# Performance work log

Measured on AMD Instinct MI355X. Metric: run time of the kernel, lower is better.

The kernel has to match this reference:

```python
import jax, jax.numpy as jnp
import numpy as np

N_NODES = 50000
N_EDGES = 800000
ND = 64   # node_dim
HD = 128  # hidden_dim
ED = 32   # edge_dim


def setup_inputs() -> dict:
    key = jax.random.key(0)
    ks = jax.random.split(key, 16)
    init = lambda k, shape: (jax.random.normal(k, shape, jnp.float32)
                             / np.float32(np.sqrt(shape[0])))
    h = jax.random.normal(ks[0], (N_NODES, ND), jnp.float32)
    x = jax.random.normal(ks[1], (N_NODES, 3), jnp.float32) * 10.0
    edge_index = jax.random.randint(ks[2], (2, N_EDGES), 0, N_NODES, dtype=jnp.int64)
    # realistic edge distances = actual pairwise distances of sampled edges
    edge_dist = jnp.linalg.norm(x[edge_index[0]] - x[edge_index[1]], axis=-1)
    in_dim = 2 * ND + ED
    return {
        "h": h, "x": x, "edge_index": edge_index, "edge_dist": edge_dist,
        # edge_mlp: Linear(1, ED) -> SiLU -> Linear(ED, ED)
        "We1": init(ks[3], (1, ED)), "be1": jnp.zeros((ED,), jnp.float32),
        "We2": init(ks[4], (ED, ED)), "be2": jnp.zeros((ED,), jnp.float32),
        # node_mlp: Linear(in_dim, HD) -> SiLU -> Linear(HD, ND)
        "Wn1": init(ks[5], (in_dim, HD)), "bn1": jnp.zeros((HD,), jnp.float32),
        "Wn2": init(ks[6], (HD, ND)), "bn2": jnp.zeros((ND,), jnp.float32),
        # coord_mlp: Linear(in_dim, HD) -> SiLU -> Linear(HD, 1, bias=False)
        "Wc1": init(ks[7], (in_dim, HD)), "bc1": jnp.zeros((HD,), jnp.float32),
        "Wc2": init(ks[8], (HD, 1)),
    }


def reference(h, x, edge_index, edge_dist,
              We1, be1, We2, be2,
              Wn1, bn1, Wn2, bn2,
              Wc1, bc1, Wc2):
    n = h.shape[0]
    src, dst = edge_index[0], edge_index[1]
    # edge_mlp on scalar distance -> [E, ED]
    e = jax.nn.silu(edge_dist[:, None] @ We1 + be1) @ We2 + be2
    # gather + concat -> [E, 2*ND + ED]
    m_input = jnp.concatenate([h[src], h[dst], e], axis=-1)
    # node messages [E, ND]
    m = jax.nn.silu(m_input @ Wn1 + bn1) @ Wn2 + bn2
    h_agg = jax.ops.segment_sum(m, dst, num_segments=n)
    # coord update weight [E, 1]
    coord_weight = jax.nn.silu(m_input @ Wc1 + bc1) @ Wc2
    dir_vec = x[src] - x[dst]
    dir_len = jnp.clip(jnp.linalg.norm(dir_vec, axis=-1, keepdims=True), 1e-8)
    coord_update = coord_weight * (dir_vec / dir_len)
    x_agg = jax.ops.segment_sum(coord_update, dst, num_segments=n)
    return h + h_agg, x + x_agg
```

## Files before the change

### kernel.cpp

```cpp
#include <hip/hip_runtime.h>


#define NN 50000
#define NE 800000
#define NDIM 64
#define HDIM 128
#define EDIM 32
#define NTILES (NE / 64)
#define MSTRIDE 168
#define HSTRIDE 136
#define MLSTRIDE 65
#define NH (NN * NDIM)
#define NX (NN * 3)

#define WS_WN1P 0
#define WS_WC1P 20480
#define WS_BN1P 40960
#define WS_BC1P 41088
#define WS_WEIGHTS_FLOATS 65536
#define NCNT 50176
#define IOFF_CNT    WS_WEIGHTS_FLOATS
#define IOFF_BLK    (IOFF_CNT + NCNT)
#define IOFF_CUR    (IOFF_BLK + 256)
#define IOFF_SRCS   (IOFF_CUR + NCNT)
#define IOFF_DSTS   (IOFF_SRCS + NE)
#define IOFF_DISTS  (IOFF_DSTS + NE)
#define WS_TOTAL_BYTES ((size_t)(IOFF_DISTS + NE) * 4)

typedef __bf16 bf16x8 __attribute__((ext_vector_type(8)));
typedef float f32x4 __attribute__((ext_vector_type(4)));
typedef unsigned short ushort8 __attribute__((ext_vector_type(8)));
typedef unsigned short ushort4v __attribute__((ext_vector_type(4)));

__device__ __forceinline__ unsigned short f2bf(float f) {
    union { __bf16 b; unsigned short u; } c;
    c.b = (__bf16)f;
    return c.u;
}
__device__ __forceinline__ float silu(float v) {
    return __fdividef(v, 1.0f + __expf(-v));
}

__device__ __forceinline__ void bar_lds() {
    asm volatile("s_waitcnt lgkmcnt(0)" ::: "memory");
    __builtin_amdgcn_s_barrier();
}

__device__ __forceinline__ bf16x8 ld_frag(const unsigned short* p) {
    union { ushort8 u; bf16x8 v; } c;
    c.u = *(const ushort8*)p;
    return c.v;
}
__device__ __forceinline__ bf16x8 mk_frag(const unsigned short* u) {
    union { ushort8 uu; bf16x8 v; } c;
#pragma unroll
    for (int j = 0; j < 8; ++j) c.uu[j] = u[j];
    return c.v;
}

__global__ void init_out(const float* __restrict__ h, const float* __restrict__ x,
                         float* __restrict__ out) {
    int i = blockIdx.x * 256 + threadIdx.x;
    if (i < NH) out[i] = h[i];
    else if (i < NH + NX) out[i] = x[i - NH];
}


__global__ __launch_bounds__(256) void zero_cnt(int* __restrict__ cnt, int* __restrict__ cur) {
    const int i = blockIdx.x * 256 + threadIdx.x;
    if (i < NCNT) { cnt[i] = 0; cur[i] = 0; }
}

__global__ __launch_bounds__(256) void hist_dst(const int* __restrict__ dst, int* __restrict__ cnt) {
    const int e = blockIdx.x * 256 + threadIdx.x;
    if (e < NE) atomicAdd(&cnt[dst[e]], 1);
}

__global__ __launch_bounds__(256) void scan1(int* __restrict__ cnt, int* __restrict__ blk) {
    __shared__ int sh[256];
    const int t = threadIdx.x, i = blockIdx.x * 256 + t;
    const int v = cnt[i];
    sh[t] = v;
    __syncthreads();
#pragma unroll
    for (int d = 1; d < 256; d <<= 1) {
        const int o = (t >= d) ? sh[t - d] : 0;
        __syncthreads();
        sh[t] += o;
        __syncthreads();
    }
    cnt[i] = sh[t] - v;
    if (t == 255) blk[blockIdx.x] = sh[t];
}

__global__ __launch_bounds__(256) void scan2(int* __restrict__ blk) {
    __shared__ int sh[256];
    const int t = threadIdx.x;
    const int v = (t < 196) ? blk[t] : 0;
    sh[t] = v;
    __syncthreads();
#pragma unroll
    for (int d = 1; d < 256; d <<= 1) {
        const int o = (t >= d) ? sh[t - d] : 0;
        __syncthreads();
        sh[t] += o;
        __syncthreads();
    }
    if (t < 196) blk[t] = sh[t] - v;
}

__global__ __launch_bounds__(256) void scan3(int* __restrict__ cnt, const int* __restrict__ blk) {
    const int i = blockIdx.x * 256 + threadIdx.x;
    if (i < NCNT) cnt[i] += blk[blockIdx.x];
}

__global__ __launch_bounds__(256) void scatter_edges(
    const int* __restrict__ src, const int* __restrict__ dst,
    const float* __restrict__ dist,
    const int* __restrict__ base, int* __restrict__ cur,
    int* __restrict__ srcs, int* __restrict__ dsts, float* __restrict__ dists) {
    const int e = blockIdx.x * 256 + threadIdx.x;
    if (e < NE) {
        const int d = dst[e];
        const int pos = base[d] + atomicAdd(&cur[d], 1);
        srcs[pos] = src[e];
        dsts[pos] = d;
        dists[pos] = dist[e];
    }
}


__global__ __launch_bounds__(128) void fold_weights(
    const float* __restrict__ We2, const float* __restrict__ be2,
    const float* __restrict__ Wn1, const float* __restrict__ bn1,
    const float* __restrict__ Wc1, const float* __restrict__ bc1,
    float* __restrict__ ws) {
    const int b = blockIdx.x;
    const int col = threadIdx.x;
    if (b < 320) {
        const int path = (b >= 160);
        const float* W = path ? Wc1 : Wn1;
        float* Wp = ws + (path ? WS_WC1P : WS_WN1P);
        const int r = path ? (b - 160) : b;
        if (r < 128) {
            Wp[r * 128 + col] = W[r * 128 + col];
        } else {
            const int j = r - 128;
            float s = 0.0f;
#pragma unroll
            for (int n = 0; n < 32; ++n)
                s += We2[j * 32 + n] * W[(128 + n) * 128 + col];
            Wp[r * 128 + col] = s;
        }
    } else {
        const int path = b - 320;
        const float* W = path ? Wc1 : Wn1;
        const float* bb = path ? bc1 : bn1;
        float* bp = ws + (path ? WS_BC1P : WS_BN1P);
        float s = bb[col];
#pragma unroll
        for (int n = 0; n < 32; ++n)
            s += be2[n] * W[(128 + n) * 128 + col];
        bp[col] = s;
    }
}


__global__ __launch_bounds__(256, 2) void egnn_edges(
    const float* __restrict__ h, const float* __restrict__ x,
    const int* __restrict__ srcg, const int* __restrict__ dstg,
    const float* __restrict__ dist,
    const float* __restrict__ We1, const float* __restrict__ be1,
    const float* __restrict__ Wn2, const float* __restrict__ bn2,
    const float* __restrict__ Wc2,
    const float* __restrict__ wsW,
    float* __restrict__ outh, float* __restrict__ outx) {

    __shared__ __align__(16) unsigned short mlds[64 * MSTRIDE];
    __shared__ __align__(16) unsigned short hl[64 * HSTRIDE];
    __shared__ int src_l[64];
    __shared__ int dst_l[64];
    __shared__ float we1_l[32], be1_l[32];
    __shared__ float part_l[256];
    __shared__ float cx_l[64], cy_l[64], cz_l[64];

    const int tid  = threadIdx.x;
    const int w    = tid >> 6;
    const int lane = tid & 63;
    const int l15  = lane & 15;
    const int quad = lane >> 4;

    const float* Wn1p = wsW + WS_WN1P;
    const float* Wc1p = wsW + WS_WC1P;
    const float* bn1p = wsW + WS_BN1P;
    const float* bc1p = wsW + WS_BC1P;

    if (tid < 32) { we1_l[tid] = We1[tid]; be1_l[tid] = be1[tid]; }

    bf16x8 wn1f[5][2], wc1f[5][2];
#pragma unroll
    for (int kc = 0; kc < 5; ++kc) {
#pragma unroll
        for (int nt = 0; nt < 2; ++nt) {
            unsigned short un[8], uc[8];
            const int n = w * 32 + nt * 16 + l15;
#pragma unroll
            for (int j = 0; j < 8; ++j) {
                const int k = kc * 32 + quad * 8 + j;
                un[j] = f2bf(Wn1p[k * HDIM + n]);
                uc[j] = f2bf(Wc1p[k * HDIM + n]);
            }
            wn1f[kc][nt] = mk_frag(un);
            wc1f[kc][nt] = mk_frag(uc);
        }
    }
    bf16x8 wn2f[4];
#pragma unroll
    for (int kc = 0; kc < 4; ++kc) {
        unsigned short u[8];
        const int n = w * 16 + l15;
#pragma unroll
        for (int j = 0; j < 8; ++j) {
            const int k = kc * 32 + quad * 8 + j;
            u[j] = f2bf(Wn2[k * NDIM + n]);
        }
        wn2f[kc] = mk_frag(u);
    }
    const float biasN0 = bn1p[w * 32 + l15];
    const float biasN1 = bn1p[w * 32 + 16 + l15];
    const float biasC0 = bc1p[w * 32 + l15];
    const float biasC1 = bc1p[w * 32 + 16 + l15];
    const float bias2v = bn2[w * 16 + l15];
    const float wcA = Wc2[w * 32 + l15];
    const float wcB = Wc2[w * 32 + 16 + l15];

    for (int tile = blockIdx.x; tile < NTILES; tile += gridDim.x) {
        int pf_s = 0, pf_d = 0;
        if (tid < 64) {
            const int e = tile * 64 + tid;
            pf_s = srcg[e];
            pf_d = dstg[e];
        }
        bar_lds();

        if (tid < 64) { src_l[tid] = pf_s; dst_l[tid] = pf_d; }
        bar_lds();

        {
            const int c4 = tid & 15, sub = tid >> 4;
#pragma unroll
            for (int it = 0; it < 4; ++it) {
                const int el = sub + it * 16;
                const float4 hs = *(const float4*)(h + (size_t)src_l[el] * NDIM + c4 * 4);
                const float4 hd = *(const float4*)(h + (size_t)dst_l[el] * NDIM + c4 * 4);
                ushort4v us = { f2bf(hs.x), f2bf(hs.y), f2bf(hs.z), f2bf(hs.w) };
                ushort4v ud = { f2bf(hd.x), f2bf(hd.y), f2bf(hd.z), f2bf(hd.w) };
                *(ushort4v*)&mlds[el * MSTRIDE + c4 * 4] = us;
                *(ushort4v*)&mlds[el * MSTRIDE + 64 + c4 * 4] = ud;
            }
        }
        {
            const int el = tid >> 2, j0 = (tid & 3) * 8;
            const float dv = dist[tile * 64 + el];
            ushort8 u;
#pragma unroll
            for (int j = 0; j < 8; ++j)
                u[j] = f2bf(silu(dv * we1_l[j0 + j] + be1_l[j0 + j]));
            *(ushort8*)&mlds[el * MSTRIDE + 128 + j0] = u;
        }
        bar_lds();

        f32x4 accN[4][2], accC[4][2];
#pragma unroll
        for (int mt = 0; mt < 4; ++mt) {
            accN[mt][0] = (f32x4){biasN0, biasN0, biasN0, biasN0};
            accN[mt][1] = (f32x4){biasN1, biasN1, biasN1, biasN1};
            accC[mt][0] = (f32x4){biasC0, biasC0, biasC0, biasC0};
            accC[mt][1] = (f32x4){biasC1, biasC1, biasC1, biasC1};
        }
#pragma unroll
        for (int kc = 0; kc < 5; ++kc) {
            bf16x8 af[4];
#pragma unroll
            for (int mt = 0; mt < 4; ++mt)
                af[mt] = ld_frag(&mlds[(mt * 16 + l15) * MSTRIDE + kc * 32 + quad * 8]);
#pragma unroll
            for (int mt = 0; mt < 4; ++mt) {
#pragma unroll
                for (int nt = 0; nt < 2; ++nt) {
                    accN[mt][nt] = __builtin_amdgcn_mfma_f32_16x16x32_bf16(
                        af[mt], wn1f[kc][nt], accN[mt][nt], 0, 0, 0);
                    accC[mt][nt] = __builtin_amdgcn_mfma_f32_16x16x32_bf16(
                        af[mt], wc1f[kc][nt], accC[mt][nt], 0, 0, 0);
                }
            }
        }

#pragma unroll
        for (int mt = 0; mt < 4; ++mt)
#pragma unroll
            for (int nt = 0; nt < 2; ++nt)
#pragma unroll
                for (int r = 0; r < 4; ++r)
                    hl[(mt * 16 + quad * 4 + r) * HSTRIDE + w * 32 + nt * 16 + l15] =
                        f2bf(silu(accN[mt][nt][r]));

        {
            float p[16];
#pragma unroll
            for (int mt = 0; mt < 4; ++mt)
#pragma unroll
                for (int r = 0; r < 4; ++r)
                    p[mt * 4 + r] = silu(accC[mt][0][r]) * wcA + silu(accC[mt][1][r]) * wcB;

            float q8[8];
#pragma unroll
            for (int i = 0; i < 8; ++i) {
                const float send = (l15 & 8) ? p[i] : p[i + 8];
                const float recv = __shfl_xor(send, 8, 64);
                q8[i] = ((l15 & 8) ? p[i + 8] : p[i]) + recv;
            }
            float q4[4];
#pragma unroll
            for (int i = 0; i < 4; ++i) {
                const float send = (l15 & 4) ? q8[i] : q8[i + 4];
                const float recv = __shfl_xor(send, 4, 64);
                q4[i] = ((l15 & 4) ? q8[i + 4] : q8[i]) + recv;
            }
            float q2[2];
#pragma unroll
            for (int i = 0; i < 2; ++i) {
                const float send = (l15 & 2) ? q4[i] : q4[i + 2];
                const float recv = __shfl_xor(send, 2, 64);
                q2[i] = ((l15 & 2) ? q4[i + 2] : q4[i]) + recv;
            }
            {
                const float send = (l15 & 1) ? q2[0] : q2[1];
                const float recv = __shfl_xor(send, 1, 64);
                const float tot = ((l15 & 1) ? q2[1] : q2[0]) + recv;
                const int edge = (l15 >> 2) * 16 + quad * 4 + (l15 & 3);
                part_l[w * 64 + edge] = tot;
            }
        }
        bar_lds();

        f32x4 acc2[4];
#pragma unroll
        for (int mt = 0; mt < 4; ++mt) acc2[mt] = (f32x4){bias2v, bias2v, bias2v, bias2v};
#pragma unroll
        for (int kc = 0; kc < 4; ++kc) {
#pragma unroll
            for (int mt = 0; mt < 4; ++mt) {
                bf16x8 a2 = ld_frag(&hl[(mt * 16 + l15) * HSTRIDE + kc * 32 + quad * 8]);
                acc2[mt] = __builtin_amdgcn_mfma_f32_16x16x32_bf16(a2, wn2f[kc], acc2[mt], 0, 0, 0);
            }
        }

        {
            float* ml = (float*)mlds;
#pragma unroll
            for (int mt = 0; mt < 4; ++mt)
#pragma unroll
                for (int r = 0; r < 4; ++r)
                    ml[(mt * 16 + quad * 4 + r) * MLSTRIDE + w * 16 + l15] = acc2[mt][r];
        }

        if (tid < 64) {
            const float cw = part_l[tid] + part_l[64 + tid] + part_l[128 + tid] + part_l[192 + tid];
            const int sn = src_l[tid], dn = dst_l[tid];
            const float dx = x[sn * 3 + 0] - x[dn * 3 + 0];
            const float dy = x[sn * 3 + 1] - x[dn * 3 + 1];
            const float dz = x[sn * 3 + 2] - x[dn * 3 + 2];
            float len = sqrtf(dx * dx + dy * dy + dz * dz);
            len = fmaxf(len, 1e-8f);
            const float f = cw / len;
            cx_l[tid] = f * dx; cy_l[tid] = f * dy; cz_l[tid] = f * dz;
        }
        bar_lds();

        {
            const int c = lane, g = w;
            const int r0 = g * 16;
            float acc = ((const float*)mlds)[r0 * MLSTRIDE + c];
            int d = dst_l[r0];
#pragma unroll
            for (int r = r0 + 1; r < r0 + 16; ++r) {
                const int dn = dst_l[r];
                if (dn != d) {
                    atomicAdd(outh + (size_t)d * NDIM + c, acc);
                    acc = 0.0f;
                    d = dn;
                }
                acc += ((const float*)mlds)[r * MLSTRIDE + c];
            }
            atomicAdd(outh + (size_t)d * NDIM + c, acc);
        }

        if (tid < 64) {
            const int d = dst_l[tid];
            if (tid == 0 || dst_l[tid - 1] != d) {
                float sx = 0.0f, sy = 0.0f, sz = 0.0f;
                int r = tid;
                do {
                    sx += cx_l[r]; sy += cy_l[r]; sz += cz_l[r];
                    ++r;
                } while (r < 64 && dst_l[r] == d);
                atomicAdd(outx + (size_t)d * 3 + 0, sx);
                atomicAdd(outx + (size_t)d * 3 + 1, sy);
                atomicAdd(outx + (size_t)d * 3 + 2, sz);
            }
        }
    }
}

extern "C" void kernel_launch(void* const* d_in, const int* in_sizes, int n_in,
                              void* d_out, int out_size, void* d_ws, size_t ws_size,
                              hipStream_t stream) {
    const float* h    = (const float*)d_in[0];
    const float* x    = (const float*)d_in[1];
    const int*   ei   = (const int*)d_in[2];
    const float* dist = (const float*)d_in[3];
    const float* We1  = (const float*)d_in[4];
    const float* be1  = (const float*)d_in[5];
    const float* We2  = (const float*)d_in[6];
    const float* be2  = (const float*)d_in[7];
    const float* Wn1  = (const float*)d_in[8];
    const float* bn1  = (const float*)d_in[9];
    const float* Wn2  = (const float*)d_in[10];
    const float* bn2  = (const float*)d_in[11];
    const float* Wc1  = (const float*)d_in[12];
    const float* bc1  = (const float*)d_in[13];
    const float* Wc2  = (const float*)d_in[14];

    float* outh = (float*)d_out;
    float* outx = outh + (size_t)NH;
    float* ws   = (float*)d_ws;

    fold_weights<<<322, 128, 0, stream>>>(We2, be2, Wn1, bn1, Wc1, bc1, ws);
    init_out<<<(NH + NX + 255) / 256, 256, 0, stream>>>(h, x, (float*)d_out);

    const int* es = ei;
    const int* ed = ei + NE;
    const float* edist = dist;

    if (ws_size >= WS_TOTAL_BYTES) {
        int*   cnt   = (int*)d_ws + IOFF_CNT;
        int*   blk   = (int*)d_ws + IOFF_BLK;
        int*   cur   = (int*)d_ws + IOFF_CUR;
        int*   srcs  = (int*)d_ws + IOFF_SRCS;
        int*   dsts  = (int*)d_ws + IOFF_DSTS;
        float* dists = (float*)((int*)d_ws + IOFF_DISTS);

        zero_cnt<<<NCNT / 256, 256, 0, stream>>>(cnt, cur);
        hist_dst<<<NE / 256, 256, 0, stream>>>(ed, cnt);
        scan1<<<NCNT / 256, 256, 0, stream>>>(cnt, blk);
        scan2<<<1, 256, 0, stream>>>(blk);
        scan3<<<NCNT / 256, 256, 0, stream>>>(cnt, blk);
        scatter_edges<<<NE / 256, 256, 0, stream>>>(es, ed, dist, cnt, cur,
                                                    srcs, dsts, dists);
        es = srcs; ed = dsts; edist = dists;
    }

    egnn_edges<<<1024, 256, 0, stream>>>(h, x, es, ed, edist,
                                         We1, be1, Wn2, bn2, Wc2, ws,
                                         outh, outx);
}
```

Measured before the change: 458.0 us.

## Fuse preprocessing kernels into one persistent prep kernel with grid sync

Replaces the weight-fold, output init, zeroing, histogram, three-stage scan and scatter kernels with a single 512-block kernel that separates its phases with atomic-counter grid barriers, plus one memset. The main edge kernel splits the node and coord first-layer MFMA loops so fewer accumulators are live, raises the occupancy hint to 3 blocks per SM, and uses a grid of 768. It also drops the separate index staging barrier by reading edge indices straight from global memory. The software grid barrier assumes all 512 blocks are resident at once and can deadlock if they are not. The extra occupancy may force register spills.

```diff
diff --git a/kernel.cpp b/kernel.cpp
--- a/kernel.cpp
+++ b/kernel.cpp
@@ -5,7 +5,6 @@
 #define NE 800000
 #define NDIM 64
 #define HDIM 128
-#define EDIM 32
 #define NTILES (NE / 64)
 #define MSTRIDE 168
 #define HSTRIDE 136
@@ -20,12 +19,17 @@
 #define WS_WEIGHTS_FLOATS 65536
 #define NCNT 50176
 #define IOFF_CNT    WS_WEIGHTS_FLOATS
-#define IOFF_BLK    (IOFF_CNT + NCNT)
-#define IOFF_CUR    (IOFF_BLK + 256)
-#define IOFF_SRCS   (IOFF_CUR + NCNT)
+#define IOFF_CUR    (IOFF_CNT + NCNT)
+#define IOFF_SYNC   (IOFF_CUR + NCNT)
+#define IOFF_BLK    (IOFF_SYNC + 64)
+#define IOFF_SRCS   (IOFF_BLK + 256)
 #define IOFF_DSTS   (IOFF_SRCS + NE)
 #define IOFF_DISTS  (IOFF_DSTS + NE)
 #define WS_TOTAL_BYTES ((size_t)(IOFF_DISTS + NE) * 4)
+#define MEMSET_OFF_BYTES ((size_t)IOFF_CNT * 4)
+#define MEMSET_BYTES ((size_t)(2 * NCNT + 64 + 256) * 4)
+
+#define PREP_NB 512
 
 typedef __bf16 bf16x8 __attribute__((ext_vector_type(8)));
 typedef float f32x4 __attribute__((ext_vector_type(4)));
@@ -40,12 +44,10 @@
 __device__ __forceinline__ float silu(float v) {
     return __fdividef(v, 1.0f + __expf(-v));
 }
-
 __device__ __forceinline__ void bar_lds() {
     asm volatile("s_waitcnt lgkmcnt(0)" ::: "memory");
     __builtin_amdgcn_s_barrier();
 }
-
 __device__ __forceinline__ bf16x8 ld_frag(const unsigned short* p) {
     union { ushort8 u; bf16x8 v; } c;
     c.u = *(const ushort8*)p;
@@ -58,115 +60,129 @@
     return c.v;
 }
 
-__global__ void init_out(const float* __restrict__ h, const float* __restrict__ x,
-                         float* __restrict__ out) {
-    int i = blockIdx.x * 256 + threadIdx.x;
-    if (i < NH) out[i] = h[i];
-    else if (i < NH + NX) out[i] = x[i - NH];
-}
-
-
-__global__ __launch_bounds__(256) void zero_cnt(int* __restrict__ cnt, int* __restrict__ cur) {
-    const int i = blockIdx.x * 256 + threadIdx.x;
-    if (i < NCNT) { cnt[i] = 0; cur[i] = 0; }
-}
-
-__global__ __launch_bounds__(256) void hist_dst(const int* __restrict__ dst, int* __restrict__ cnt) {
-    const int e = blockIdx.x * 256 + threadIdx.x;
-    if (e < NE) atomicAdd(&cnt[dst[e]], 1);
-}
-
-__global__ __launch_bounds__(256) void scan1(int* __restrict__ cnt, int* __restrict__ blk) {
-    __shared__ int sh[256];
-    const int t = threadIdx.x, i = blockIdx.x * 256 + t;
-    const int v = cnt[i];
-    sh[t] = v;
+
+__device__ __forceinline__ void gsync(int* sc) {
     __syncthreads();
-#pragma unroll
-    for (int d = 1; d < 256; d <<= 1) {
-        const int o = (t >= d) ? sh[t - d] : 0;
-        __syncthreads();
-        sh[t] += o;
-        __syncthreads();
-    }
-    cnt[i] = sh[t] - v;
-    if (t == 255) blk[blockIdx.x] = sh[t];
-}
-
-__global__ __launch_bounds__(256) void scan2(int* __restrict__ blk) {
-    __shared__ int sh[256];
-    const int t = threadIdx.x;
-    const int v = (t < 196) ? blk[t] : 0;
-    sh[t] = v;
+    if (threadIdx.x == 0) {
+        __threadfence();
+        atomicAdd(sc, 1);
+        while (__hip_atomic_load(sc, __ATOMIC_RELAXED, __HIP_MEMORY_SCOPE_AGENT) < PREP_NB)
+            __builtin_amdgcn_s_sleep(2);
+        __threadfence();
+    }
     __syncthreads();
-#pragma unroll
-    for (int d = 1; d < 256; d <<= 1) {
-        const int o = (t >= d) ? sh[t - d] : 0;
-        __syncthreads();
-        sh[t] += o;
-        __syncthreads();
-    }
-    if (t < 196) blk[t] = sh[t] - v;
-}
-
-__global__ __launch_bounds__(256) void scan3(int* __restrict__ cnt, const int* __restrict__ blk) {
-    const int i = blockIdx.x * 256 + threadIdx.x;
-    if (i < NCNT) cnt[i] += blk[blockIdx.x];
-}
-
-__global__ __launch_bounds__(256) void scatter_edges(
-    const int* __restrict__ src, const int* __restrict__ dst,
-    const float* __restrict__ dist,
-    const int* __restrict__ base, int* __restrict__ cur,
-    int* __restrict__ srcs, int* __restrict__ dsts, float* __restrict__ dists) {
-    const int e = blockIdx.x * 256 + threadIdx.x;
-    if (e < NE) {
-        const int d = dst[e];
-        const int pos = base[d] + atomicAdd(&cur[d], 1);
-        srcs[pos] = src[e];
-        dsts[pos] = d;
-        dists[pos] = dist[e];
-    }
-}
-
-
-__global__ __launch_bounds__(128) void fold_weights(
+}
+
+__global__ __launch_bounds__(256) void prep(
+    const float* __restrict__ h, const float* __restrict__ x,
+    const int* __restrict__ src0, const int* __restrict__ dst0,
+    const float* __restrict__ dist0,
     const float* __restrict__ We2, const float* __restrict__ be2,
     const float* __restrict__ Wn1, const float* __restrict__ bn1,
     const float* __restrict__ Wc1, const float* __restrict__ bc1,
-    float* __restrict__ ws) {
-    const int b = blockIdx.x;
-    const int col = threadIdx.x;
-    if (b < 320) {
-        const int path = (b >= 160);
-        const float* W = path ? Wc1 : Wn1;
-        float* Wp = ws + (path ? WS_WC1P : WS_WN1P);
-        const int r = path ? (b - 160) : b;
-        if (r < 128) {
-            Wp[r * 128 + col] = W[r * 128 + col];
+    float* __restrict__ out, int* __restrict__ wsi, int do_sort) {
+
+    __shared__ int sh[256];
+    const int gtid = blockIdx.x * 256 + threadIdx.x;
+    const int G = PREP_NB * 256;
+
+    float* wsf = (float*)wsi;
+    int* cnt  = wsi + IOFF_CNT;
+    int* cur  = wsi + IOFF_CUR;
+    int* sync = wsi + IOFF_SYNC;
+    int* blk  = wsi + IOFF_BLK;
+
+    for (int i = gtid; i < 41216; i += G) {
+        if (i < 40960) {
+            const int path = i / 20480;
+            const int rem = i - path * 20480;
+            const int r = rem >> 7, col = rem & 127;
+            const float* W = path ? Wc1 : Wn1;
+            float* Wp = wsf + (path ? WS_WC1P : WS_WN1P);
+            if (r < 128) {
+                Wp[r * 128 + col] = W[r * 128 + col];
+            } else {
+                const int j = r - 128;
+                float s = 0.0f;
+#pragma unroll
+                for (int n = 0; n < 32; ++n)
+                    s += We2[j * 32 + n] * W[(128 + n) * 128 + col];
+                Wp[r * 128 + col] = s;
+            }
         } else {
-            const int j = r - 128;
-            float s = 0.0f;
+            const int j = i - 40960;
+            const int path = j >> 7, col = j & 127;
+            const float* W = path ? Wc1 : Wn1;
+            const float* bb = path ? bc1 : bn1;
+            float s = bb[col];
 #pragma unroll
             for (int n = 0; n < 32; ++n)
-                s += We2[j * 32 + n] * W[(128 + n) * 128 + col];
-            Wp[r * 128 + col] = s;
-        }
-    } else {
-        const int path = b - 320;
-        const float* W = path ? Wc1 : Wn1;
-        const float* bb = path ? bc1 : bn1;
-        float* bp = ws + (path ? WS_BC1P : WS_BN1P);
-        float s = bb[col];
-#pragma unroll
-        for (int n = 0; n < 32; ++n)
-            s += be2[n] * W[(128 + n) * 128 + col];
-        bp[col] = s;
-    }
-}
-
-
-__global__ __launch_bounds__(256, 2) void egnn_edges(
+                s += be2[n] * W[(128 + n) * 128 + col];
+            wsf[(path ? WS_BC1P : WS_BN1P) + col] = s;
+        }
+    }
+    for (int i = gtid; i < NH + NX; i += G)
+        out[i] = (i < NH) ? h[i] : x[i - NH];
+
+    if (!do_sort) return;
+
+    gsync(&sync[0]);
+
+    for (int e = gtid; e < NE; e += G)
+        atomicAdd(&cnt[dst0[e]], 1);
+
+    gsync(&sync[16]);
+
+    if (blockIdx.x < 196) {
+        const int t = threadIdx.x;
+        const int i = blockIdx.x * 256 + t;
+        const int v = cnt[i];
+        sh[t] = v;
+        __syncthreads();
+#pragma unroll
+        for (int d = 1; d < 256; d <<= 1) {
+            const int o = (t >= d) ? sh[t - d] : 0;
+            __syncthreads();
+            sh[t] += o;
+            __syncthreads();
+        }
+        cnt[i] = sh[t] - v;
+        if (t == 255) blk[blockIdx.x] = sh[t];
+    }
+
+    gsync(&sync[32]);
+
+    if (blockIdx.x == 0) {
+        const int t = threadIdx.x;
+        const int v = (t < 196) ? blk[t] : 0;
+        sh[t] = v;
+        __syncthreads();
+#pragma unroll
+        for (int d = 1; d < 256; d <<= 1) {
+            const int o = (t >= d) ? sh[t - d] : 0;
+            __syncthreads();
+            sh[t] += o;
+            __syncthreads();
+        }
+        if (t < 196) blk[t] = sh[t] - v;
+    }
+
+    gsync(&sync[48]);
+
+    int* srcs = wsi + IOFF_SRCS;
+    int* dsts = wsi + IOFF_DSTS;
+    float* dists = (float*)(wsi + IOFF_DISTS);
+    for (int e = gtid; e < NE; e += G) {
+        const int d = dst0[e];
+        const int pos = cnt[d] + blk[d >> 8] + atomicAdd(&cur[d], 1);
+        srcs[pos] = src0[e];
+        dsts[pos] = d;
+        dists[pos] = dist0[e];
+    }
+}
+
+
+__global__ __launch_bounds__(256, 3) void egnn_edges(
     const float* __restrict__ h, const float* __restrict__ x,
     const int* __restrict__ srcg, const int* __restrict__ dstg,
     const float* __restrict__ dist,
@@ -235,24 +251,19 @@
     const float wcB = Wc2[w * 32 + 16 + l15];
 
     for (int tile = blockIdx.x; tile < NTILES; tile += gridDim.x) {
-        int pf_s = 0, pf_d = 0;
-        if (tid < 64) {
-            const int e = tile * 64 + tid;
-            pf_s = srcg[e];
-            pf_d = dstg[e];
-        }
+        const int e0 = tile * 64;
         bar_lds();
 
-        if (tid < 64) { src_l[tid] = pf_s; dst_l[tid] = pf_d; }
-        bar_lds();
-
+        if (tid < 64) { src_l[tid] = srcg[e0 + tid]; dst_l[tid] = dstg[e0 + tid]; }
         {
             const int c4 = tid & 15, sub = tid >> 4;
 #pragma unroll
             for (int it = 0; it < 4; ++it) {
                 const int el = sub + it * 16;
-                const float4 hs = *(const float4*)(h + (size_t)src_l[el] * NDIM + c4 * 4);
-                const float4 hd = *(const float4*)(h + (size_t)dst_l[el] * NDIM + c4 * 4);
+                const int sn = srcg[e0 + el];
+                const int dn = dstg[e0 + el];
+                const float4 hs = *(const float4*)(h + (size_t)sn * NDIM + c4 * 4);
+                const float4 hd = *(const float4*)(h + (size_t)dn * NDIM + c4 * 4);
                 ushort4v us = { f2bf(hs.x), f2bf(hs.y), f2bf(hs.z), f2bf(hs.w) };
                 ushort4v ud = { f2bf(hd.x), f2bf(hd.y), f2bf(hd.z), f2bf(hd.w) };
                 *(ushort4v*)&mlds[el * MSTRIDE + c4 * 4] = us;
@@ -261,7 +272,7 @@
         }
         {
             const int el = tid >> 2, j0 = (tid & 3) * 8;
-            const float dv = dist[tile * 64 + el];
+            const float dv = dist[e0 + el];
             ushort8 u;
 #pragma unroll
             for (int j = 0; j < 8; ++j)
@@ -270,42 +281,48 @@
         }
         bar_lds();
 
-        f32x4 accN[4][2], accC[4][2];
-#pragma unroll
-        for (int mt = 0; mt < 4; ++mt) {
-            accN[mt][0] = (f32x4){biasN0, biasN0, biasN0, biasN0};
-            accN[mt][1] = (f32x4){biasN1, biasN1, biasN1, biasN1};
-            accC[mt][0] = (f32x4){biasC0, biasC0, biasC0, biasC0};
-            accC[mt][1] = (f32x4){biasC1, biasC1, biasC1, biasC1};
-        }
-#pragma unroll
-        for (int kc = 0; kc < 5; ++kc) {
-            bf16x8 af[4];
+        {
+            f32x4 accN[4][2];
+#pragma unroll
+            for (int mt = 0; mt < 4; ++mt) {
+                accN[mt][0] = (f32x4){biasN0, biasN0, biasN0, biasN0};
+                accN[mt][1] = (f32x4){biasN1, biasN1, biasN1, biasN1};
+            }
+#pragma unroll
+            for (int kc = 0; kc < 5; ++kc) {
+#pragma unroll
+                for (int mt = 0; mt < 4; ++mt) {
+                    bf16x8 af = ld_frag(&mlds[(mt * 16 + l15) * MSTRIDE + kc * 32 + quad * 8]);
+                    accN[mt][0] = __builtin_amdgcn_mfma_f32_16x16x32_bf16(af, wn1f[kc][0], accN[mt][0], 0, 0, 0);
+                    accN[mt][1] = __builtin_amdgcn_mfma_f32_16x16x32_bf16(af, wn1f[kc][1], accN[mt][1], 0, 0, 0);
+                }
+            }
 #pragma unroll
             for (int mt = 0; mt < 4; ++mt)
-                af[mt] = ld_frag(&mlds[(mt * 16 + l15) * MSTRIDE + kc * 32 + quad * 8]);
+#pragma unroll
+                for (int nt = 0; nt < 2; ++nt)
+#pragma unroll
+                    for (int r = 0; r < 4; ++r)
+                        hl[(mt * 16 + quad * 4 + r) * HSTRIDE + w * 32 + nt * 16 + l15] =
+                            f2bf(silu(accN[mt][nt][r]));
+        }
+
+        {
+            f32x4 accC[4][2];
 #pragma unroll
             for (int mt = 0; mt < 4; ++mt) {
-#pragma unroll
-                for (int nt = 0; nt < 2; ++nt) {
-                    accN[mt][nt] = __builtin_amdgcn_mfma_f32_16x16x32_bf16(
-                        af[mt], wn1f[kc][nt], accN[mt][nt], 0, 0, 0);
-                    accC[mt][nt] = __builtin_amdgcn_mfma_f32_16x16x32_bf16(
-                        af[mt], wc1f[kc][nt], accC[mt][nt], 0, 0, 0);
+                accC[mt][0] = (f32x4){biasC0, biasC0, biasC0, biasC0};
+                accC[mt][1] = (f32x4){biasC1, biasC1, biasC1, biasC1};
+            }
+#pragma unroll
+            for (int kc = 0; kc < 5; ++kc) {
+#pragma unroll
+                for (int mt = 0; mt < 4; ++mt) {
+                    bf16x8 af = ld_frag(&mlds[(mt * 16 + l15) * MSTRIDE + kc * 32 + quad * 8]);
+                    accC[mt][0] = __builtin_amdgcn_mfma_f32_16x16x32_bf16(af, wc1f[kc][0], accC[mt][0], 0, 0, 0);
+                    accC[mt][1] = __builtin_amdgcn_mfma_f32_16x16x32_bf16(af, wc1f[kc][1], accC[mt][1], 0, 0, 0);
                 }
             }
-        }
-
-#pragma unroll
-        for (int mt = 0; mt < 4; ++mt)
-#pragma unroll
-            for (int nt = 0; nt < 2; ++nt)
-#pragma unroll
-                for (int r = 0; r < 4; ++r)
-                    hl[(mt * 16 + quad * 4 + r) * HSTRIDE + w * 32 + nt * 16 + l15] =
-                        f2bf(silu(accN[mt][nt][r]));
-
-        {
             float p[16];
 #pragma unroll
             for (int mt = 0; mt < 4; ++mt)
@@ -344,19 +361,18 @@
         }
         bar_lds();
 
-        f32x4 acc2[4];
-#pragma unroll
-        for (int mt = 0; mt < 4; ++mt) acc2[mt] = (f32x4){bias2v, bias2v, bias2v, bias2v};
-#pragma unroll
-        for (int kc = 0; kc < 4; ++kc) {
-#pragma unroll
-            for (int mt = 0; mt < 4; ++mt) {
-                bf16x8 a2 = ld_frag(&hl[(mt * 16 + l15) * HSTRIDE + kc * 32 + quad * 8]);
-                acc2[mt] = __builtin_amdgcn_mfma_f32_16x16x32_bf16(a2, wn2f[kc], acc2[mt], 0, 0, 0);
-            }
-        }
-
-        {
+        {
+            f32x4 acc2[4];
+#pragma unroll
+            for (int mt = 0; mt < 4; ++mt) acc2[mt] = (f32x4){bias2v, bias2v, bias2v, bias2v};
+#pragma unroll
+            for (int kc = 0; kc < 4; ++kc) {
+#pragma unroll
+                for (int mt = 0; mt < 4; ++mt) {
+                    bf16x8 a2 = ld_frag(&hl[(mt * 16 + l15) * HSTRIDE + kc * 32 + quad * 8]);
+                    acc2[mt] = __builtin_amdgcn_mfma_f32_16x16x32_bf16(a2, wn2f[kc], acc2[mt], 0, 0, 0);
+                }
+            }
             float* ml = (float*)mlds;
 #pragma unroll
             for (int mt = 0; mt < 4; ++mt)
@@ -379,8 +395,8 @@
         bar_lds();
 
         {
-            const int c = lane, g = w;
-            const int r0 = g * 16;
+            const int c = lane;
+            const int r0 = w * 16;
             float acc = ((const float*)mlds)[r0 * MLSTRIDE + c];
             int d = dst_l[r0];
 #pragma unroll
@@ -434,34 +450,27 @@
 
     float* outh = (float*)d_out;
     float* outx = outh + (size_t)NH;
-    float* ws   = (float*)d_ws;
-
-    fold_weights<<<322, 128, 0, stream>>>(We2, be2, Wn1, bn1, Wc1, bc1, ws);
-    init_out<<<(NH + NX + 255) / 256, 256, 0, stream>>>(h, x, (float*)d_out);
+    int*   wsi  = (int*)d_ws;
+
+    const int do_sort = (ws_size >= WS_TOTAL_BYTES) ? 1 : 0;
+    if (do_sort)
+        hipMemsetAsync((char*)d_ws + MEMSET_OFF_BYTES, 0, MEMSET_BYTES, stream);
+
+    prep<<<PREP_NB, 256, 0, stream>>>(h, x, ei, ei + NE, dist,
+                                      We2, be2, Wn1, bn1, Wc1, bc1,
+                                      (float*)d_out, wsi, do_sort);
 
     const int* es = ei;
     const int* ed = ei + NE;
     const float* edist = dist;
-
-    if (ws_size >= WS_TOTAL_BYTES) {
-        int*   cnt   = (int*)d_ws + IOFF_CNT;
-        int*   blk   = (int*)d_ws + IOFF_BLK;
-        int*   cur   = (int*)d_ws + IOFF_CUR;
-        int*   srcs  = (int*)d_ws + IOFF_SRCS;
-        int*   dsts  = (int*)d_ws + IOFF_DSTS;
-        float* dists = (float*)((int*)d_ws + IOFF_DISTS);
-
-        zero_cnt<<<NCNT / 256, 256, 0, stream>>>(cnt, cur);
-        hist_dst<<<NE / 256, 256, 0, stream>>>(ed, cnt);
-        scan1<<<NCNT / 256, 256, 0, stream>>>(cnt, blk);
-        scan2<<<1, 256, 0, stream>>>(blk);
-        scan3<<<NCNT / 256, 256, 0, stream>>>(cnt, blk);
-        scatter_edges<<<NE / 256, 256, 0, stream>>>(es, ed, dist, cnt, cur,
-                                                    srcs, dsts, dists);
-        es = srcs; ed = dsts; edist = dists;
-    }
-
-    egnn_edges<<<1024, 256, 0, stream>>>(h, x, es, ed, edist,
-                                         We1, be1, Wn2, bn2, Wc2, ws,
-                                         outh, outx);
-}
+    if (do_sort) {
+        es = wsi + IOFF_SRCS;
+        ed = wsi + IOFF_DSTS;
+        edist = (const float*)(wsi + IOFF_DISTS);
+    }
+
+    egnn_edges<<<768, 256, 0, stream>>>(h, x, es, ed, edist,
+                                        We1, be1, Wn2, bn2, Wc2,
+                                        (const float*)d_ws,
+                                        outh, outx);
+}
```

After: 612.6 us. +33.7%, slower.
